# Kernel optimization log

Measured on AMD Instinct MI355X. Metric: run time of the kernel, lower is better.

The kernel has to match this reference:

```python
import jax, jax.numpy as jnp
import numpy as np

B, N, D = 8, 2048, 512

def setup_inputs() -> dict:
    key = jax.random.key(0)
    k1, k2, k3, k4, k5 = jax.random.split(key, 5)
    s = 1.0 / np.sqrt(D)
    return {
        "x": jax.random.normal(k1, (B, N, D), dtype=jnp.float32),
        "w_qkv": jax.random.normal(k2, (D, 3 * D), dtype=jnp.float32) * s,
        "b_qkv": jax.random.normal(k3, (3 * D,), dtype=jnp.float32) * 0.01,
        "w_fc": jax.random.normal(k4, (D, D), dtype=jnp.float32) * s,
        "b_fc": jax.random.normal(k5, (D,), dtype=jnp.float32) * 0.01,
    }

def reference(x, w_qkv, b_qkv, w_fc, b_fc):
    scale = 1.0 / (x.shape[-1] ** 0.5)
    qkv = x @ w_qkv + b_qkv                      # [B, N, 3D]
    q, k, v = jnp.split(qkv, 3, axis=-1)         # each [B, N, D]
    attn = jnp.einsum("bnd,bmd->bnm", q, k) * scale
    attn = jax.nn.softmax(attn, axis=-1)
    out = jnp.einsum("bnm,bmd->bnd", attn, v)
    return out @ w_fc + b_fc + x
```

## Files before the change

### kernel.cpp

```cpp
#include <hip/hip_runtime.h>
#include <stdint.h>

typedef unsigned short u16;
typedef unsigned int u32;
typedef __attribute__((ext_vector_type(8))) short short8;
typedef __attribute__((ext_vector_type(4))) float f32x4;
typedef __attribute__((ext_vector_type(8))) unsigned short u16x8;
typedef __attribute__((ext_vector_type(4))) float float4_t;

__device__ __forceinline__ float b2f(u16 u) { return __uint_as_float(((u32)u) << 16); }
__device__ __forceinline__ u16 f2b(float f) {
  u32 u = __float_as_uint(f);
  u += 0x7fffu + ((u >> 16) & 1u);
  return (u16)(u >> 16);
}

typedef const __attribute__((address_space(1))) void* gas_t;
typedef __attribute__((address_space(3))) void* las_t;
__device__ __forceinline__ void gl_lds16(const void* g, void* l) {
  __builtin_amdgcn_global_load_lds((gas_t)(uintptr_t)g, (las_t)(u32)(uintptr_t)l, 16, 0, 0);
}
__device__ __forceinline__ void barrier_pin() {
  __builtin_amdgcn_sched_barrier(0);
  __builtin_amdgcn_s_barrier();
  __builtin_amdgcn_sched_barrier(0);
}
__device__ __forceinline__ void lgkm0_pin() {
  asm volatile("s_waitcnt lgkmcnt(0)" ::: "memory");
  __builtin_amdgcn_sched_barrier(0);
}

__global__ __launch_bounds__(256) void cvt_f2b_kernel(const float* __restrict__ src,
                                                      u16* __restrict__ dst, long n) {
  long i = ((long)blockIdx.x * 256 + threadIdx.x) * 8;
  if (i >= n) return;
  float4_t v0 = *(const float4_t*)(src + i);
  float4_t v1 = *(const float4_t*)(src + i + 4);
  u16x8 o;
#pragma unroll
  for (int j = 0; j < 4; ++j) { o[j] = f2b(v0[j]); o[4 + j] = f2b(v1[j]); }
  *(u16x8*)(dst + i) = o;
}

__global__ __launch_bounds__(256) void tr_cvt(const float* __restrict__ src,
                                              u16* __restrict__ dst, int R, int C) {
  __shared__ float t[32][33];
  const int bx = blockIdx.x * 32;
  const int by = blockIdx.y * 32;
  const int tx = threadIdx.x & 31, ty = threadIdx.x >> 5;
#pragma unroll
  for (int i = 0; i < 32; i += 8)
    t[ty + i][tx] = src[(long)(by + ty + i) * C + bx + tx];
  __syncthreads();
#pragma unroll
  for (int i = 0; i < 32; i += 8)
    dst[(long)(bx + ty + i) * R + by + tx] = f2b(t[tx][ty + i]);
}

__global__ __launch_bounds__(256) void tr_v(const u16* __restrict__ qkv, u16* __restrict__ vt) {
  __shared__ u16 t[32][33];
  const int b = blockIdx.z;
  const int r0 = blockIdx.x * 32;
  const int d0 = blockIdx.y * 32;
  const int tx = threadIdx.x & 31, ty = threadIdx.x >> 5;
#pragma unroll
  for (int i = 0; i < 32; i += 8)
    t[ty + i][tx] = qkv[((long)b * 2048 + r0 + ty + i) * 1536 + 1024 + d0 + tx];
  __syncthreads();
#pragma unroll
  for (int i = 0; i < 32; i += 8)
    vt[((long)b * 512 + d0 + ty + i) * 2048 + r0 + tx] = t[tx][ty + i];
}

template <bool OUT_F32, bool BIAS, bool RES>
__global__ __launch_bounds__(512, 4)
void gemm128(const u16* __restrict__ A, const u16* __restrict__ Bt, void* __restrict__ Cv,
             const float* __restrict__ bias, const float* __restrict__ res,
             int K, int lda, int ldb, int ldc,
             long aStride, long bStride, long cStride, float alpha) {
  __shared__ u16 As[2][128 * 64];
  __shared__ u16 Bs[2][128 * 64];
  const int tid = threadIdx.x;
  const int wid = tid >> 6, lane = tid & 63;
  const int wr = wid >> 2, wc = wid & 3;
  const int lr = lane & 15, lg = lane >> 4;

  const int gx = gridDim.x, gy = gridDim.y;
  int id = (blockIdx.z * gy + blockIdx.y) * gx + blockIdx.x;
  const int nwg = gx * gy * gridDim.z;
  id = (id & 7) * (nwg >> 3) + (id >> 3);
  const int bxi = id % gx;
  const int t2 = id / gx;
  const int byi = t2 % gy;
  const long z = t2 / gy;

  A += z * aStride;
  Bt += z * bStride;
  const int by = byi * 128;
  const int bx = bxi * 128;

  f32x4 acc[4][2] = {};
  short8 ah[4][2], bh[2][2];

  const int w8l = wid * 8 + (lane >> 3);
  const int scol_src = ((lane & 7) ^ (lane >> 3)) * 8;
  const int scol_lin = (lane & 7) * 8;
  const int nT = K >> 6;
  const int sx = lane & 7;

  auto stage = [&](int kt) {
    const int bb = kt & 1;
    const long kc = (long)kt * 64 + scol_src;
#pragma unroll
    for (int r = 0; r < 2; ++r) {
      const int row = r * 64 + w8l;
      gl_lds16(A + (long)(by + row) * lda + kc, &As[bb][row * 64 + scol_lin]);
    }
#pragma unroll
    for (int r = 0; r < 2; ++r) {
      const int row = r * 64 + w8l;
      gl_lds16(Bt + (long)(bx + row) * ldb + kc, &Bs[bb][row * 64 + scol_lin]);
    }
  };

  stage(0);
  asm volatile("s_waitcnt vmcnt(0)" ::: "memory");
  barrier_pin();

  for (int T = 0; T < nT; ++T) {
    const int bb = T & 1;
    const bool more = (T + 1) < nT;
    if (more) stage(T + 1);
#pragma unroll
    for (int mi = 0; mi < 4; ++mi)
#pragma unroll
      for (int ks = 0; ks < 2; ++ks)
        ah[mi][ks] = *(const short8*)&As[bb][(wr * 64 + mi * 16 + lr) * 64 +
                                             (((ks * 4 + lg) ^ sx) * 8)];
#pragma unroll
    for (int n = 0; n < 2; ++n)
#pragma unroll
      for (int ks = 0; ks < 2; ++ks)
        bh[n][ks] = *(const short8*)&Bs[bb][(wc * 32 + n * 16 + lr) * 64 +
                                            (((ks * 4 + lg) ^ sx) * 8)];
    lgkm0_pin();
    __builtin_amdgcn_s_setprio(1);
#pragma unroll
    for (int mi = 0; mi < 4; ++mi)
#pragma unroll
      for (int n = 0; n < 2; ++n)
#pragma unroll
        for (int ks = 0; ks < 2; ++ks)
          acc[mi][n] = __builtin_amdgcn_mfma_f32_16x16x32_bf16(
              ah[mi][ks], bh[n][ks], acc[mi][n], 0, 0, 0);
    __builtin_amdgcn_s_setprio(0);
    if (more) asm volatile("s_waitcnt vmcnt(0)" ::: "memory");
    barrier_pin();
  }

  if constexpr (OUT_F32) {
    float* C = (float*)Cv + z * cStride;
#pragma unroll
    for (int mi = 0; mi < 4; ++mi)
#pragma unroll
      for (int ni = 0; ni < 2; ++ni)
#pragma unroll
        for (int j = 0; j < 4; ++j) {
          const long row = by + wr * 64 + mi * 16 + lg * 4 + j;
          const int col = bx + wc * 32 + ni * 16 + lr;
          float v = acc[mi][ni][j] * alpha;
          if (BIAS) v += bias[col];
          if (RES) v += res[row * (long)ldc + col];
          C[row * (long)ldc + col] = v;
        }
  } else {
    u16* C = (u16*)Cv + z * cStride;
#pragma unroll
    for (int mi = 0; mi < 4; ++mi)
#pragma unroll
      for (int ni = 0; ni < 2; ++ni)
#pragma unroll
        for (int j = 0; j < 4; ++j) {
          const long row = by + wr * 64 + mi * 16 + lg * 4 + j;
          const int col = bx + wc * 32 + ni * 16 + lr;
          float v = acc[mi][ni][j] * alpha;
          if (BIAS) v += bias[col];
          C[row * (long)ldc + col] = f2b(v);
        }
  }
}

__global__ __launch_bounds__(256) void softmax_rows(u16* __restrict__ S) {
  const long row = blockIdx.x;
  u16* p = S + row * 2048;
  const int tid = threadIdx.x;
  const int wid = tid >> 6, lane = tid & 63;
  u16x8 v = ((const u16x8*)p)[tid];
  float f[8];
#pragma unroll
  for (int j = 0; j < 8; ++j) f[j] = b2f(v[j]);
  float m = f[0];
#pragma unroll
  for (int j = 1; j < 8; ++j) m = fmaxf(m, f[j]);
#pragma unroll
  for (int off = 32; off; off >>= 1) m = fmaxf(m, __shfl_xor(m, off));
  __shared__ float rmax[4], rsum[4];
  if (lane == 0) rmax[wid] = m;
  __syncthreads();
  m = fmaxf(fmaxf(rmax[0], rmax[1]), fmaxf(rmax[2], rmax[3]));
  float s = 0.f;
#pragma unroll
  for (int j = 0; j < 8; ++j) { f[j] = __expf(f[j] - m); s += f[j]; }
#pragma unroll
  for (int off = 32; off; off >>= 1) s += __shfl_xor(s, off);
  if (lane == 0) rsum[wid] = s;
  __syncthreads();
  s = rsum[0] + rsum[1] + rsum[2] + rsum[3];
  const float inv = 1.0f / s;
  u16x8 o;
#pragma unroll
  for (int j = 0; j < 8; ++j) o[j] = f2b(f[j] * inv);
  ((u16x8*)p)[tid] = o;
}

extern "C" void kernel_launch(void* const* d_in, const int* in_sizes, int n_in,
                              void* d_out, int out_size, void* d_ws, size_t ws_size,
                              hipStream_t stream) {
  const float* x = (const float*)d_in[0];
  const float* w_qkv = (const float*)d_in[1];
  const float* b_qkv = (const float*)d_in[2];
  const float* w_fc = (const float*)d_in[3];
  const float* b_fc = (const float*)d_in[4];
  float* out = (float*)d_out;

  char* ws = (char*)d_ws;
  const long MT = 16384;
  u16* xb = (u16*)(ws);
  u16* wqkvT = (u16*)(ws + 16777216);
  u16* wfcT = (u16*)(ws + 18350080);
  u16* qkv = (u16*)(ws + 18874368);
  u16* vt = (u16*)(ws + 69206016);
  u16* S = (u16*)(ws + 85983232);
  u16* attn = xb;

  cvt_f2b_kernel<<<4096, 256, 0, stream>>>(x, xb, MT * 512);
  tr_cvt<<<dim3(48, 16), 256, 0, stream>>>(w_qkv, wqkvT, 512, 1536);
  tr_cvt<<<dim3(16, 16), 256, 0, stream>>>(w_fc, wfcT, 512, 512);

  gemm128<false, true, false><<<dim3(12, 128, 1), 512, 0, stream>>>(
      xb, wqkvT, qkv, b_qkv, nullptr, 512, 512, 512, 1536, 0, 0, 0, 1.0f);

  tr_v<<<dim3(64, 16, 8), 256, 0, stream>>>(qkv, vt);

  gemm128<false, false, false><<<dim3(16, 16, 8), 512, 0, stream>>>(
      qkv, qkv + 512, S, nullptr, nullptr, 512, 1536, 1536, 2048,
      (long)2048 * 1536, (long)2048 * 1536, (long)2048 * 2048, 0.04419417382415922f);

  softmax_rows<<<16384, 256, 0, stream>>>(S);

  gemm128<false, false, false><<<dim3(4, 16, 8), 512, 0, stream>>>(
      S, vt, attn, nullptr, nullptr, 2048, 2048, 2048, 512,
      (long)2048 * 2048, (long)512 * 2048, (long)2048 * 512, 1.0f);

  gemm128<true, true, true><<<dim3(4, 128, 1), 512, 0, stream>>>(
      attn, wfcT, out, b_fc, x, 512, 512, 512, 512, 0, 0, 0, 1.0f);
}
```

Measured before the change: 180.0 us.

## Fuse softmax exp and row sums into QK GEMM, normalize in PV GEMM

```diff
diff --git a/kernel.cpp b/kernel.cpp
--- a/kernel.cpp
+++ b/kernel.cpp
@@ -72,14 +72,26 @@
     vt[((long)b * 512 + d0 + ty + i) * 2048 + r0 + tx] = t[tx][ty + i];
 }
 
-template <bool OUT_F32, bool BIAS, bool RES>
+__global__ __launch_bounds__(256) void sum_inv(const float* __restrict__ part,
+                                               float* __restrict__ inv_l) {
+  const int r = blockIdx.x * 256 + threadIdx.x;
+  const float* p = part + (long)r * 16;
+  float s = 0.f;
+#pragma unroll
+  for (int i = 0; i < 16; ++i) s += p[i];
+  inv_l[r] = 1.0f / s;
+}
+
+template <bool OUT_F32, bool BIAS, bool RES, bool EXPSUM, bool DIVL>
 __global__ __launch_bounds__(512, 4)
 void gemm128(const u16* __restrict__ A, const u16* __restrict__ Bt, void* __restrict__ Cv,
              const float* __restrict__ bias, const float* __restrict__ res,
+             float* __restrict__ part, const float* __restrict__ inv_l,
              int K, int lda, int ldb, int ldc,
              long aStride, long bStride, long cStride, float alpha) {
   __shared__ u16 As[2][128 * 64];
   __shared__ u16 Bs[2][128 * 64];
+  __shared__ float lsum[EXPSUM ? 4 : 1][EXPSUM ? 128 : 1];
   const int tid = threadIdx.x;
   const int wid = tid >> 6, lane = tid & 63;
   const int wr = wid >> 2, wc = wid & 3;
@@ -158,7 +170,29 @@
     barrier_pin();
   }
 
-  if constexpr (OUT_F32) {
+  if constexpr (EXPSUM) {
+    u16* C = (u16*)Cv + z * cStride;
+#pragma unroll
+    for (int mi = 0; mi < 4; ++mi) {
+#pragma unroll
+      for (int j = 0; j < 4; ++j) {
+        const long row = by + wr * 64 + mi * 16 + lg * 4 + j;
+        float e0 = __expf(acc[mi][0][j] * alpha);
+        float e1 = __expf(acc[mi][1][j] * alpha);
+        C[row * (long)ldc + bx + wc * 32 + 0 * 16 + lr] = f2b(e0);
+        C[row * (long)ldc + bx + wc * 32 + 1 * 16 + lr] = f2b(e1);
+        float t = e0 + e1;
+#pragma unroll
+        for (int off = 1; off < 16; off <<= 1) t += __shfl_xor(t, off);
+        if (lr == 0) lsum[wc][wr * 64 + mi * 16 + lg * 4 + j] = t;
+      }
+    }
+    __syncthreads();
+    if (tid < 128) {
+      const float s = lsum[0][tid] + lsum[1][tid] + lsum[2][tid] + lsum[3][tid];
+      part[(z * 2048 + by + tid) * 16 + bxi] = s;
+    }
+  } else if constexpr (OUT_F32) {
     float* C = (float*)Cv + z * cStride;
 #pragma unroll
     for (int mi = 0; mi < 4; ++mi)
@@ -184,43 +218,11 @@
           const long row = by + wr * 64 + mi * 16 + lg * 4 + j;
           const int col = bx + wc * 32 + ni * 16 + lr;
           float v = acc[mi][ni][j] * alpha;
+          if (DIVL) v *= inv_l[z * 2048 + by + wr * 64 + mi * 16 + lg * 4 + j];
           if (BIAS) v += bias[col];
           C[row * (long)ldc + col] = f2b(v);
         }
   }
-}
-
-__global__ __launch_bounds__(256) void softmax_rows(u16* __restrict__ S) {
-  const long row = blockIdx.x;
-  u16* p = S + row * 2048;
-  const int tid = threadIdx.x;
-  const int wid = tid >> 6, lane = tid & 63;
-  u16x8 v = ((const u16x8*)p)[tid];
-  float f[8];
-#pragma unroll
-  for (int j = 0; j < 8; ++j) f[j] = b2f(v[j]);
-  float m = f[0];
-#pragma unroll
-  for (int j = 1; j < 8; ++j) m = fmaxf(m, f[j]);
-#pragma unroll
-  for (int off = 32; off; off >>= 1) m = fmaxf(m, __shfl_xor(m, off));
-  __shared__ float rmax[4], rsum[4];
-  if (lane == 0) rmax[wid] = m;
-  __syncthreads();
-  m = fmaxf(fmaxf(rmax[0], rmax[1]), fmaxf(rmax[2], rmax[3]));
-  float s = 0.f;
-#pragma unroll
-  for (int j = 0; j < 8; ++j) { f[j] = __expf(f[j] - m); s += f[j]; }
-#pragma unroll
-  for (int off = 32; off; off >>= 1) s += __shfl_xor(s, off);
-  if (lane == 0) rsum[wid] = s;
-  __syncthreads();
-  s = rsum[0] + rsum[1] + rsum[2] + rsum[3];
-  const float inv = 1.0f / s;
-  u16x8 o;
-#pragma unroll
-  for (int j = 0; j < 8; ++j) o[j] = f2b(f[j] * inv);
-  ((u16x8*)p)[tid] = o;
 }
 
 extern "C" void kernel_launch(void* const* d_in, const int* in_sizes, int n_in,
@@ -242,26 +244,32 @@
   u16* vt = (u16*)(ws + 69206016);
   u16* S = (u16*)(ws + 85983232);
   u16* attn = xb;
+  float* part = (float*)(ws + 16777216);
+  float* inv_l = (float*)(ws + 16777216 + 1048576);
 
   cvt_f2b_kernel<<<4096, 256, 0, stream>>>(x, xb, MT * 512);
   tr_cvt<<<dim3(48, 16), 256, 0, stream>>>(w_qkv, wqkvT, 512, 1536);
   tr_cvt<<<dim3(16, 16), 256, 0, stream>>>(w_fc, wfcT, 512, 512);
 
-  gemm128<false, true, false><<<dim3(12, 128, 1), 512, 0, stream>>>(
-      xb, wqkvT, qkv, b_qkv, nullptr, 512, 512, 512, 1536, 0, 0, 0, 1.0f);
+  gemm128<false, true, false, false, false><<<dim3(12, 128, 1), 512, 0, stream>>>(
+      xb, wqkvT, qkv, b_qkv, nullptr, nullptr, nullptr,
+      512, 512, 512, 1536, 0, 0, 0, 1.0f);
 
   tr_v<<<dim3(64, 16, 8), 256, 0, stream>>>(qkv, vt);
 
-  gemm128<false, false, false><<<dim3(16, 16, 8), 512, 0, stream>>>(
-      qkv, qkv + 512, S, nullptr, nullptr, 512, 1536, 1536, 2048,
+  gemm128<false, false, false, true, false><<<dim3(16, 16, 8), 512, 0, stream>>>(
+      qkv, qkv + 512, S, nullptr, nullptr, part, nullptr,
+      512, 1536, 1536, 2048,
       (long)2048 * 1536, (long)2048 * 1536, (long)2048 * 2048, 0.04419417382415922f);
 
-  softmax_rows<<<16384, 256, 0, stream>>>(S);
-
-  gemm128<false, false, false><<<dim3(4, 16, 8), 512, 0, stream>>>(
-      S, vt, attn, nullptr, nullptr, 2048, 2048, 2048, 512,
+  sum_inv<<<64, 256, 0, stream>>>(part, inv_l);
+
+  gemm128<false, false, false, false, true><<<dim3(4, 16, 8), 512, 0, stream>>>(
+      S, vt, attn, nullptr, nullptr, nullptr, inv_l,
+      2048, 2048, 2048, 512,
       (long)2048 * 2048, (long)512 * 2048, (long)2048 * 512, 1.0f);
 
-  gemm128<true, true, true><<<dim3(4, 128, 1), 512, 0, stream>>>(
-      attn, wfcT, out, b_fc, x, 512, 512, 512, 512, 0, 0, 0, 1.0f);
-}
+  gemm128<true, true, true, false, false><<<dim3(4, 128, 1), 512, 0, stream>>>(
+      attn, wfcT, out, b_fc, x, nullptr, nullptr,
+      512, 512, 512, 512, 0, 0, 0, 1.0f);
+}
```

New measurement: 173.2 us. -3.8%, faster.
